# Performance work log

Measured on AMD Instinct MI355X. Metric: run time of the kernel, lower is better.

## Reference

```python
import jax, jax.numpy as jnp
import numpy as np

N = 32768      # total nodes (512 graphs x 64 padded nodes)
E = 262144     # edges (avg degree 8)
F_IN = 74      # atom feature dim
D0 = 128       # dim_embedding
D1 = 256       # hidden feats
B = 512        # batch_size (graphs)
NPG = 64       # nodes per graph
EPS = 1e-5     # BatchNorm1d eps


def setup_inputs() -> dict:
    key = jax.random.key(0)
    ks = jax.random.split(key, 8)
    def rn(k, shape, s=0.05):
        return jax.random.normal(k, shape, jnp.float32) * s
    # init_transform weight [D0, F_IN]; padding=True zeroes the last row
    W_init = rn(ks[0], (D0, F_IN)).at[-1].set(0.0)
    return {
        "node_feats": jax.random.normal(ks[1], (N, F_IN), jnp.float32),
        "W_init": W_init,
        "gcn_w1": rn(ks[2], (D0, D1)), "gcn_b1": jnp.zeros((D1,), jnp.float32),
        "res_w1": rn(ks[3], (D1, D0)), "res_b1": jnp.zeros((D1,), jnp.float32),
        "bn_g1": jnp.ones((D1,), jnp.float32), "bn_b1": jnp.zeros((D1,), jnp.float32),
        "gcn_w2": rn(ks[4], (D1, D1)), "gcn_b2": jnp.zeros((D1,), jnp.float32),
        "bn_g2": jnp.ones((D1,), jnp.float32), "bn_b2": jnp.zeros((D1,), jnp.float32),
        "edge_src": jax.random.randint(ks[5], (E,), 0, N),
        "edge_dst": jax.random.randint(ks[6], (E,), 0, N),
    }


def _agg(x, src, dst):
    # DGL GraphConv norm='both': D_out^{-1/2} gather-scatter D_in^{-1/2}, degrees clamped to >= 1
    ones = jnp.ones((src.shape[0],), x.dtype)
    deg_out = jnp.clip(jax.ops.segment_sum(ones, src, num_segments=N), 1.0)
    deg_in = jnp.clip(jax.ops.segment_sum(ones, dst, num_segments=N), 1.0)
    xs = x * jax.lax.rsqrt(deg_out)[:, None]
    agg = jax.ops.segment_sum(xs[src], dst, num_segments=N)  # [N, d]
    return agg * jax.lax.rsqrt(deg_in)[:, None]


def _bn(x, g, b):
    # BatchNorm1d training-mode: batch stats over node axis, biased var
    m = x.mean(0)
    v = x.var(0)
    return (x - m) * jax.lax.rsqrt(v + EPS) * g + b


def reference(node_feats, W_init, gcn_w1, gcn_b1, res_w1, res_b1, bn_g1, bn_b1,
              gcn_w2, gcn_b2, bn_g2, bn_b2, edge_src, edge_dst):
    h = node_feats @ W_init.T  # [N, D0]
    # layer 1: residual Linear 128->256, GCN(aggregate then weight, since in<out), GELU, BN
    res = h @ res_w1.T + res_b1
    g = jax.nn.gelu(_agg(h, edge_src, edge_dst) @ gcn_w1 + gcn_b1, approximate=False)
    h = _bn(g + res, bn_g1, bn_b1)
    # layer 2: Identity residual
    g = jax.nn.gelu(_agg(h, edge_src, edge_dst) @ gcn_w2 + gcn_b2, approximate=False)
    h = _bn(g + h, bn_g2, bn_b2)
    return h.reshape(B, NPG, D1)
```

## Files before the change

### kernel.cpp

```cpp
#include <hip/hip_runtime.h>
#include <hip/hip_bf16.h>
#include <math.h>

#define N_NODES 32768
#define E_EDGES 262144
#define F_INF   74
#define KP      96
#define D0      128
#define D1      256
#define BN_EPS  1e-5f
#define RBLK    1024

#if __has_builtin(__builtin_amdgcn_cvt_pk_f32_fp8)
#define HW_FP8 1
#else
#define HW_FP8 0
#endif

typedef float f32x4 __attribute__((ext_vector_type(4)));
typedef float f32x2 __attribute__((ext_vector_type(2)));
typedef short s16x8 __attribute__((ext_vector_type(8)));

__device__ __forceinline__ float b2f(ushort h) { return __uint_as_float(((unsigned)h) << 16); }
__device__ __forceinline__ ushort f2b(float f) {
    unsigned u = __float_as_uint(f);
    return (ushort)((u + 0x7FFFu + ((u >> 16) & 1u)) >> 16);
}
__device__ __forceinline__ unsigned char f2q(float f) {
    unsigned u = __float_as_uint(f * 7.52316384526264005e-37f);
    unsigned s = (u >> 24) & 0x80u;
    int r = (int)(((u & 0x7fffffffu) + 0x80000u) >> 20);
    r = r > 126 ? 126 : r;
    return (unsigned char)(s | (unsigned)r);
}
__device__ __forceinline__ float q2f(unsigned x) {
    unsigned fb = ((x & 0x80u) << 24) | ((x & 0x7fu) << 20);
    return __uint_as_float(fb) * 1.32922799578491587e+36f;
}
__device__ __forceinline__ void acc8(float* a, uint2 v, float c) {
#if HW_FP8
    f32x2 p;
    p = __builtin_amdgcn_cvt_pk_f32_fp8((int)v.x, false); a[0] += p[0] * c; a[1] += p[1] * c;
    p = __builtin_amdgcn_cvt_pk_f32_fp8((int)v.x, true);  a[2] += p[0] * c; a[3] += p[1] * c;
    p = __builtin_amdgcn_cvt_pk_f32_fp8((int)v.y, false); a[4] += p[0] * c; a[5] += p[1] * c;
    p = __builtin_amdgcn_cvt_pk_f32_fp8((int)v.y, true);  a[6] += p[0] * c; a[7] += p[1] * c;
#else
    unsigned d;
    d = v.x; a[0] += q2f(d & 255u) * c; a[1] += q2f((d >> 8) & 255u) * c;
             a[2] += q2f((d >> 16) & 255u) * c; a[3] += q2f(d >> 24) * c;
    d = v.y; a[4] += q2f(d & 255u) * c; a[5] += q2f((d >> 8) & 255u) * c;
             a[6] += q2f((d >> 16) & 255u) * c; a[7] += q2f(d >> 24) * c;
#endif
}
__device__ __forceinline__ float gelu_exact(float x) {
    return 0.5f * x * (1.0f + erff(x * 0.70710678118654752440f));
}


__global__ void k_front_a(const int* __restrict__ src, const int* __restrict__ dst,
                          int* __restrict__ deg,
                          const float* __restrict__ nf, const float* __restrict__ Wi,
                          const float* __restrict__ w1, const float* __restrict__ rw,
                          const float* __restrict__ w2,
                          ushort* __restrict__ nfB, ushort* __restrict__ WTB,
                          ushort* __restrict__ WB1, ushort* __restrict__ RWB,
                          ushort* __restrict__ WB2) {
    int bid = blockIdx.x;
    int tid = threadIdx.x;
    if (bid < 1024) {
        int e = bid * 256 + tid;
        atomicAdd(&deg[src[e]], 1);
        atomicAdd(&deg[N_NODES + dst[e]], 1);
        return;
    }
    int idx = (bid - 1024) * 256 + tid;
    {
        int n = idx / KP, k = idx - n * KP;
        nfB[idx] = (k < F_INF) ? f2b(nf[n * F_INF + k]) : (ushort)0;
    }
    if (idx < D0 * KP) {
        int c = idx / KP, k = idx - c * KP;
        WTB[idx] = (k < F_INF) ? f2b(Wi[c * F_INF + k]) : (ushort)0;
    }
    if (idx < D1 * D0) {
        int n = idx >> 7, k = idx & 127;
        WB1[idx] = f2b(w1[k * D1 + n]);
        RWB[idx] = f2b(rw[idx]);
    }
    if (idx < D1 * D1) {
        int n = idx >> 8, k = idx & 255;
        WB2[idx] = f2b(w2[k * D1 + n]);
    }
}

__global__ __launch_bounds__(1024) void k_scan(const int* __restrict__ deg,
                                               int* __restrict__ row_off,
                                               float* __restrict__ rsq_out,
                                               float* __restrict__ rsq_in,
                                               int* __restrict__ cursor) {
    __shared__ int part[1024];
    int t = threadIdx.x;
    int base = t * 32;
    int loc[32];
    int s = 0;
    #pragma unroll
    for (int i = 0; i < 32; i++) { loc[i] = s; s += deg[N_NODES + base + i]; }
    part[t] = s;
    #pragma unroll
    for (int i = 0; i < 32; i++) {
        int n = base + i;
        int d_o = deg[n];           if (d_o < 1) d_o = 1;
        int d_i = deg[N_NODES + n]; if (d_i < 1) d_i = 1;
        rsq_out[n] = 1.0f / sqrtf((float)d_o);
        rsq_in[n]  = 1.0f / sqrtf((float)d_i);
        cursor[n] = 0;
    }
    __syncthreads();
    for (int off = 1; off < 1024; off <<= 1) {
        int v = 0;
        if (t >= off) v = part[t - off];
        __syncthreads();
        if (t >= off) part[t] += v;
        __syncthreads();
    }
    int pre = (t == 0) ? 0 : part[t - 1];
    #pragma unroll
    for (int i = 0; i < 32; i++) row_off[base + i] = pre + loc[i];
    if (t == 1023) row_off[N_NODES] = part[1023];
}


__global__ __launch_bounds__(512) void k_front_b(
    const int* __restrict__ src, const int* __restrict__ dst,
    const int* __restrict__ row_off, const float* __restrict__ rsq_out,
    int* __restrict__ cursor, int2* __restrict__ csr,
    const ushort* __restrict__ nfB, const ushort* __restrict__ WTB,
    ushort* __restrict__ h0) {
    int bid = blockIdx.x;
    int tid = threadIdx.x;
    if (bid < 512) {
        int e = bid * 512 + tid;
        int d = dst[e];
        int s = src[e];
        int slot = atomicAdd(&cursor[d], 1);
        int pos = row_off[d] + slot;
        csr[pos] = make_int2(s, __float_as_int(rsq_out[s]));
        return;
    }
    int b2 = bid - 512;
    int w = tid >> 6, lane = tid & 63, m = lane & 15, g4 = lane >> 4;
    int col = w * 16 + m;
    int rbase = b2 * 16;
    s16x8 B[3], A[3];
    #pragma unroll
    for (int j = 0; j < 3; j++)
        B[j] = *reinterpret_cast<const s16x8*>(&WTB[(size_t)col * KP + j * 32 + g4 * 8]);
    #pragma unroll
    for (int j = 0; j < 3; j++)
        A[j] = *reinterpret_cast<const s16x8*>(&nfB[(size_t)(rbase + m) * KP + j * 32 + g4 * 8]);
    f32x4 acc = (f32x4){0.f, 0.f, 0.f, 0.f};
    #pragma unroll
    for (int j = 0; j < 3; j++)
        acc = __builtin_amdgcn_mfma_f32_16x16x32_bf16(A[j], B[j], acc, 0, 0, 0);
    #pragma unroll
    for (int r = 0; r < 4; r++)
        h0[(size_t)(rbase + g4 * 4 + r) * D0 + col] = f2b(acc[r]);
}


__global__ __launch_bounds__(512) void k_layer1f(
    const ushort* __restrict__ h0B, const float* __restrict__ rsq_in,
    const int* __restrict__ row_off, const int2* __restrict__ csr,
    const ushort* __restrict__ WB1, const ushort* __restrict__ RWB,
    const float* __restrict__ b1, const float* __restrict__ rb,
    ushort* __restrict__ t1B, unsigned char* __restrict__ t1Q,
    float* __restrict__ partials) {
    __shared__ ushort sA[32 * 128];
    int tid = threadIdx.x;
    int rbase = blockIdx.x * 32;
    {
        int nloc = tid >> 4;
        int half = (tid >> 3) & 1;
        int node = rbase + nloc;
        int f = (tid & 7) * 8;
        int beg = row_off[node], end = row_off[node + 1];
        float a0[8], a1[8];
        #pragma unroll
        for (int j = 0; j < 8; j++) { a0[j] = 0.f; a1[j] = 0.f; }
        int e = beg + half;
        for (; e + 6 < end; e += 8) {
            int2 r0 = csr[e], r1 = csr[e + 2], r2 = csr[e + 4], r3 = csr[e + 6];
            float c0 = __int_as_float(r0.y), c1 = __int_as_float(r1.y);
            float c2 = __int_as_float(r2.y), c3 = __int_as_float(r3.y);
            s16x8 v00 = *reinterpret_cast<const s16x8*>(&h0B[(size_t)r0.x * D0 + f]);
            s16x8 v01 = *reinterpret_cast<const s16x8*>(&h0B[(size_t)r0.x * D0 + f + 64]);
            s16x8 v10 = *reinterpret_cast<const s16x8*>(&h0B[(size_t)r1.x * D0 + f]);
            s16x8 v11 = *reinterpret_cast<const s16x8*>(&h0B[(size_t)r1.x * D0 + f + 64]);
            s16x8 v20 = *reinterpret_cast<const s16x8*>(&h0B[(size_t)r2.x * D0 + f]);
            s16x8 v21 = *reinterpret_cast<const s16x8*>(&h0B[(size_t)r2.x * D0 + f + 64]);
            s16x8 v30 = *reinterpret_cast<const s16x8*>(&h0B[(size_t)r3.x * D0 + f]);
            s16x8 v31 = *reinterpret_cast<const s16x8*>(&h0B[(size_t)r3.x * D0 + f + 64]);
            #pragma unroll
            for (int j = 0; j < 8; j++) {
                a0[j] += b2f((ushort)v00[j]) * c0 + b2f((ushort)v10[j]) * c1 +
                         b2f((ushort)v20[j]) * c2 + b2f((ushort)v30[j]) * c3;
                a1[j] += b2f((ushort)v01[j]) * c0 + b2f((ushort)v11[j]) * c1 +
                         b2f((ushort)v21[j]) * c2 + b2f((ushort)v31[j]) * c3;
            }
        }
        for (; e < end; e += 2) {
            int2 r = csr[e];
            float sc = __int_as_float(r.y);
            s16x8 v0 = *reinterpret_cast<const s16x8*>(&h0B[(size_t)r.x * D0 + f]);
            s16x8 v1 = *reinterpret_cast<const s16x8*>(&h0B[(size_t)r.x * D0 + f + 64]);
            #pragma unroll
            for (int j = 0; j < 8; j++) {
                a0[j] += b2f((ushort)v0[j]) * sc;
                a1[j] += b2f((ushort)v1[j]) * sc;
            }
        }
        #pragma unroll
        for (int j = 0; j < 8; j++) {
            a0[j] += __shfl_xor(a0[j], 8);
            a1[j] += __shfl_xor(a1[j], 8);
        }
        if (half == 0) {
            float si = rsq_in[node];
            s16x8 o0, o1;
            #pragma unroll
            for (int j = 0; j < 8; j++) {
                o0[j] = (short)f2b(a0[j] * si);
                o1[j] = (short)f2b(a1[j] * si);
            }
            int swz = (nloc & 15) << 4;
            int x0 = f * 2;
            *reinterpret_cast<s16x8*>(((char*)sA) + nloc * 256 + (x0 ^ swz)) = o0;
            *reinterpret_cast<s16x8*>(((char*)sA) + nloc * 256 + ((x0 + 128) ^ swz)) = o1;
        }
    }
    __syncthreads();
    int w = tid >> 6, lane = tid & 63, m = lane & 15, g4 = lane >> 4;
    int cb = w * 32;
    s16x8 BG[2][4], BR[2][4];
    #pragma unroll
    for (int nt = 0; nt < 2; nt++)
        #pragma unroll
        for (int j = 0; j < 4; j++) {
            BG[nt][j] = *reinterpret_cast<const s16x8*>(&WB1[(size_t)(cb + nt * 16 + m) * D0 + j * 32 + g4 * 8]);
            BR[nt][j] = *reinterpret_cast<const s16x8*>(&RWB[(size_t)(cb + nt * 16 + m) * D0 + j * 32 + g4 * 8]);
        }
    float bg[2], brv[2];
    #pragma unroll
    for (int nt = 0; nt < 2; nt++) {
        bg[nt]  = b1[cb + nt * 16 + m];
        brv[nt] = rb[cb + nt * 16 + m];
    }
    float ps[2] = {0.f, 0.f}, pq[2] = {0.f, 0.f};
    #pragma unroll
    for (int rt = 0; rt < 2; rt++) {
        int row = rt * 16 + m;
        s16x8 aA[4], aH[4];
        #pragma unroll
        for (int j = 0; j < 4; j++) {
            int boff = row * 256 + (((j * 4 + g4) * 16) ^ ((row & 15) << 4));
            aA[j] = *reinterpret_cast<const s16x8*>(((const char*)sA) + boff);
            aH[j] = *reinterpret_cast<const s16x8*>(&h0B[(size_t)(rbase + row) * D0 + j * 32 + g4 * 8]);
        }
        f32x4 accG[2], accR[2];
        #pragma unroll
        for (int nt = 0; nt < 2; nt++) {
            accG[nt] = (f32x4){0.f, 0.f, 0.f, 0.f};
            accR[nt] = (f32x4){0.f, 0.f, 0.f, 0.f};
        }
        #pragma unroll
        for (int j = 0; j < 4; j++)
            #pragma unroll
            for (int nt = 0; nt < 2; nt++) {
                accG[nt] = __builtin_amdgcn_mfma_f32_16x16x32_bf16(aA[j], BG[nt][j], accG[nt], 0, 0, 0);
                accR[nt] = __builtin_amdgcn_mfma_f32_16x16x32_bf16(aH[j], BR[nt][j], accR[nt], 0, 0, 0);
            }
        #pragma unroll
        for (int nt = 0; nt < 2; nt++) {
            int col = cb + nt * 16 + m;
            #pragma unroll
            for (int r = 0; r < 4; r++) {
                int orow = rbase + rt * 16 + g4 * 4 + r;
                float v = gelu_exact(accG[nt][r] + bg[nt]) + accR[nt][r] + brv[nt];
                t1B[(size_t)orow * D1 + col] = f2b(v);
                t1Q[(size_t)orow * D1 + col] = f2q(v);
                ps[nt] += v; pq[nt] += v * v;
            }
        }
    }
    #pragma unroll
    for (int nt = 0; nt < 2; nt++) {
        float s = ps[nt], q = pq[nt];
        s += __shfl_xor(s, 16); s += __shfl_xor(s, 32);
        q += __shfl_xor(q, 16); q += __shfl_xor(q, 32);
        if (g4 == 0) {
            int col = cb + nt * 16 + m;
            partials[(size_t)col * RBLK + blockIdx.x] = s;
            partials[(size_t)(256 + col) * RBLK + blockIdx.x] = q;
        }
    }
}


__global__ __launch_bounds__(1024) void k_layer2f(
    const ushort* __restrict__ t1B, const unsigned char* __restrict__ t1Q,
    const float* __restrict__ sc1, const float* __restrict__ sh1,
    const float* __restrict__ rsq_in,
    const int* __restrict__ row_off, const int2* __restrict__ csr,
    const ushort* __restrict__ WB2, const float* __restrict__ b2,
    ushort* __restrict__ t2B, float* __restrict__ partials) {
    __shared__ ushort sA[32 * 256];
    int tid = threadIdx.x;
    int rbase = blockIdx.x * 32;
    {
        int nloc = tid >> 5;
        int half = (tid >> 4) & 1;
        int node = rbase + nloc;
        int f0 = (tid & 15) * 8;
        int beg = row_off[node], end = row_off[node + 1];
        float a0[8], a1[8];
        #pragma unroll
        for (int j = 0; j < 8; j++) { a0[j] = 0.f; a1[j] = 0.f; }
        float ssum = 0.f;
        int e = beg + half;
        for (; e + 6 < end; e += 8) {
            int2 r0 = csr[e], r1 = csr[e + 2], r2 = csr[e + 4], r3 = csr[e + 6];
            float c0 = __int_as_float(r0.y), c1 = __int_as_float(r1.y);
            float c2 = __int_as_float(r2.y), c3 = __int_as_float(r3.y);
            uint2 qa0 = *reinterpret_cast<const uint2*>(&t1Q[(size_t)r0.x * D1 + f0]);
            uint2 qb0 = *reinterpret_cast<const uint2*>(&t1Q[(size_t)r0.x * D1 + f0 + 128]);
            uint2 qa1 = *reinterpret_cast<const uint2*>(&t1Q[(size_t)r1.x * D1 + f0]);
            uint2 qb1 = *reinterpret_cast<const uint2*>(&t1Q[(size_t)r1.x * D1 + f0 + 128]);
            uint2 qa2 = *reinterpret_cast<const uint2*>(&t1Q[(size_t)r2.x * D1 + f0]);
            uint2 qb2 = *reinterpret_cast<const uint2*>(&t1Q[(size_t)r2.x * D1 + f0 + 128]);
            uint2 qa3 = *reinterpret_cast<const uint2*>(&t1Q[(size_t)r3.x * D1 + f0]);
            uint2 qb3 = *reinterpret_cast<const uint2*>(&t1Q[(size_t)r3.x * D1 + f0 + 128]);
            ssum += c0 + c1 + c2 + c3;
            acc8(a0, qa0, c0); acc8(a1, qb0, c0);
            acc8(a0, qa1, c1); acc8(a1, qb1, c1);
            acc8(a0, qa2, c2); acc8(a1, qb2, c2);
            acc8(a0, qa3, c3); acc8(a1, qb3, c3);
        }
        for (; e < end; e += 2) {
            int2 r = csr[e];
            float sc = __int_as_float(r.y);
            uint2 qa = *reinterpret_cast<const uint2*>(&t1Q[(size_t)r.x * D1 + f0]);
            uint2 qb = *reinterpret_cast<const uint2*>(&t1Q[(size_t)r.x * D1 + f0 + 128]);
            ssum += sc;
            acc8(a0, qa, sc); acc8(a1, qb, sc);
        }
        #pragma unroll
        for (int j = 0; j < 8; j++) {
            a0[j] += __shfl_xor(a0[j], 16);
            a1[j] += __shfl_xor(a1[j], 16);
        }
        ssum += __shfl_xor(ssum, 16);
        if (half == 0) {
            float si = rsq_in[node];
            s16x8 o0, o1;
            #pragma unroll
            for (int j = 0; j < 8; j++) {
                o0[j] = (short)f2b((sc1[f0 + j] * a0[j] + sh1[f0 + j] * ssum) * si);
                o1[j] = (short)f2b((sc1[f0 + 128 + j] * a1[j] + sh1[f0 + 128 + j] * ssum) * si);
            }
            int swz = (nloc & 15) << 4;
            int b0 = nloc * 512 + ((f0 * 2) ^ swz);
            int b1_ = nloc * 512 + (((f0 + 128) * 2) ^ swz);
            *reinterpret_cast<s16x8*>(((char*)sA) + b0) = o0;
            *reinterpret_cast<s16x8*>(((char*)sA) + b1_) = o1;
        }
    }
    __syncthreads();
    int w = tid >> 6, lane = tid & 63, m = lane & 15, g4 = lane >> 4;
    int col = w * 16 + m;
    ushort rres[2][4];
    #pragma unroll
    for (int rt = 0; rt < 2; rt++)
        #pragma unroll
        for (int r = 0; r < 4; r++)
            rres[rt][r] = t1B[(size_t)(rbase + rt * 16 + g4 * 4 + r) * D1 + col];
    s16x8 BG[8];
    #pragma unroll
    for (int j = 0; j < 8; j++)
        BG[j] = *reinterpret_cast<const s16x8*>(&WB2[(size_t)col * D1 + j * 32 + g4 * 8]);
    float bg = b2[col], a1c = sc1[col], s1c = sh1[col];
    float ps = 0.f, pq = 0.f;
    #pragma unroll
    for (int rt = 0; rt < 2; rt++) {
        int row = rt * 16 + m;
        s16x8 aA[8];
        #pragma unroll
        for (int j = 0; j < 8; j++) {
            int boff = row * 512 + (((j * 4 + g4) * 16) ^ ((row & 15) << 4));
            aA[j] = *reinterpret_cast<const s16x8*>(((const char*)sA) + boff);
        }
        f32x4 acc = (f32x4){0.f, 0.f, 0.f, 0.f};
        #pragma unroll
        for (int j = 0; j < 8; j++)
            acc = __builtin_amdgcn_mfma_f32_16x16x32_bf16(aA[j], BG[j], acc, 0, 0, 0);
        #pragma unroll
        for (int r = 0; r < 4; r++) {
            int orow = rbase + rt * 16 + g4 * 4 + r;
            float h1v = fmaf(b2f(rres[rt][r]), a1c, s1c);
            float v = gelu_exact(acc[r] + bg) + h1v;
            t2B[(size_t)orow * D1 + col] = f2b(v);
            ps += v; pq += v * v;
        }
    }
    ps += __shfl_xor(ps, 16); ps += __shfl_xor(ps, 32);
    pq += __shfl_xor(pq, 16); pq += __shfl_xor(pq, 32);
    if (g4 == 0) {
        partials[(size_t)col * RBLK + blockIdx.x] = ps;
        partials[(size_t)(256 + col) * RBLK + blockIdx.x] = pq;
    }
}


__global__ __launch_bounds__(256) void k_reduce(
    const float* __restrict__ partials, const float* __restrict__ g,
    const float* __restrict__ b, float* __restrict__ sc, float* __restrict__ sh) {
    int c = blockIdx.x;
    int t = threadIdx.x;
    const float* ps = partials + (size_t)c * RBLK;
    const float* pq = partials + (size_t)(256 + c) * RBLK;
    float s = ps[t] + ps[t + 256] + ps[t + 512] + ps[t + 768];
    float q = pq[t] + pq[t + 256] + pq[t + 512] + pq[t + 768];
    __shared__ float Ls[256], Lq[256];
    Ls[t] = s; Lq[t] = q;
    __syncthreads();
    for (int o = 128; o > 0; o >>= 1) {
        if (t < o) { Ls[t] += Ls[t + o]; Lq[t] += Lq[t + o]; }
        __syncthreads();
    }
    if (t == 0) {
        float m = Ls[0] * (1.0f / (float)N_NODES);
        float var = Lq[0] * (1.0f / (float)N_NODES) - m * m;
        float a = g[c] / sqrtf(var + BN_EPS);
        sc[c] = a;
        sh[c] = b[c] - m * a;
    }
}


__global__ __launch_bounds__(256) void k_apply(
    const ushort* __restrict__ t2B, const float* __restrict__ sc,
    const float* __restrict__ sh, float* __restrict__ out) {
    int idx = blockIdx.x * 256 + threadIdx.x;
    size_t base = (size_t)idx * 8;
    int c = (int)(base & 255);
    s16x8 v = *reinterpret_cast<const s16x8*>(&t2B[base]);
    float4 o0, o1;
    o0.x = fmaf(b2f((ushort)v[0]), sc[c + 0], sh[c + 0]);
    o0.y = fmaf(b2f((ushort)v[1]), sc[c + 1], sh[c + 1]);
    o0.z = fmaf(b2f((ushort)v[2]), sc[c + 2], sh[c + 2]);
    o0.w = fmaf(b2f((ushort)v[3]), sc[c + 3], sh[c + 3]);
    o1.x = fmaf(b2f((ushort)v[4]), sc[c + 4], sh[c + 4]);
    o1.y = fmaf(b2f((ushort)v[5]), sc[c + 5], sh[c + 5]);
    o1.z = fmaf(b2f((ushort)v[6]), sc[c + 6], sh[c + 6]);
    o1.w = fmaf(b2f((ushort)v[7]), sc[c + 7], sh[c + 7]);
    *reinterpret_cast<float4*>(&out[base]) = o0;
    *reinterpret_cast<float4*>(&out[base + 4]) = o1;
}


static inline size_t align256(size_t x) { return (x + 255) & ~(size_t)255; }

extern "C" void kernel_launch(void* const* d_in, const int* in_sizes, int n_in,
                              void* d_out, int out_size, void* d_ws, size_t ws_size,
                              hipStream_t stream) {
    const float* node_feats = (const float*)d_in[0];
    const float* W_init     = (const float*)d_in[1];
    const float* gcn_w1     = (const float*)d_in[2];
    const float* gcn_b1     = (const float*)d_in[3];
    const float* res_w1     = (const float*)d_in[4];
    const float* res_b1     = (const float*)d_in[5];
    const float* bn_g1      = (const float*)d_in[6];
    const float* bn_b1      = (const float*)d_in[7];
    const float* gcn_w2     = (const float*)d_in[8];
    const float* gcn_b2     = (const float*)d_in[9];
    const float* bn_g2      = (const float*)d_in[10];
    const float* bn_b2      = (const float*)d_in[11];
    const int*   edge_src   = (const int*)d_in[12];
    const int*   edge_dst   = (const int*)d_in[13];
    float* out = (float*)d_out;

    char* p = (char*)d_ws;
    size_t off = 0;
    auto take = [&](size_t bytes) { void* r = p + off; off += align256(bytes); return r; };

    ushort* h0B   = (ushort*)take((size_t)N_NODES * D0 * 2);
    ushort* t1B   = (ushort*)take((size_t)N_NODES * D1 * 2);
    unsigned char* t1Q = (unsigned char*)take((size_t)N_NODES * D1);
    ushort* t2B   = (ushort*)take((size_t)N_NODES * D1 * 2);
    ushort* nfB   = (ushort*)take((size_t)N_NODES * KP * 2);
    ushort* WTB   = (ushort*)take((size_t)D0 * KP * 2);
    ushort* WB1   = (ushort*)take((size_t)D1 * D0 * 2);
    ushort* RWB   = (ushort*)take((size_t)D1 * D0 * 2);
    ushort* WB2   = (ushort*)take((size_t)D1 * D1 * 2);
    float*  part1 = (float*)take((size_t)2 * 256 * RBLK * 4);
    float*  part2 = (float*)take((size_t)2 * 256 * RBLK * 4);
    float*  sc1   = (float*)take(256 * 4);
    float*  sh1   = (float*)take(256 * 4);
    float*  sc2   = (float*)take(256 * 4);
    float*  sh2   = (float*)take(256 * 4);
    float*  rsq_out = (float*)take((size_t)N_NODES * 4);
    float*  rsq_in  = (float*)take((size_t)N_NODES * 4);
    int*    degi    = (int*)take((size_t)2 * N_NODES * 4);
    int*    cursor  = (int*)take((size_t)N_NODES * 4);
    int*    row_off = (int*)take((size_t)(N_NODES + 2) * 4);
    int2*   csr     = (int2*)take((size_t)E_EDGES * 8);

    hipMemsetAsync(degi, 0, (size_t)2 * N_NODES * 4, stream);

    k_front_a<<<1024 + (N_NODES * KP) / 256, 256, 0, stream>>>(
        edge_src, edge_dst, degi, node_feats, W_init, gcn_w1, res_w1, gcn_w2,
        nfB, WTB, WB1, RWB, WB2);

    k_scan<<<1, 1024, 0, stream>>>(degi, row_off, rsq_out, rsq_in, cursor);

    k_front_b<<<512 + N_NODES / 16, 512, 0, stream>>>(
        edge_src, edge_dst, row_off, rsq_out, cursor, csr, nfB, WTB, h0B);

    k_layer1f<<<RBLK, 512, 0, stream>>>(h0B, rsq_in, row_off, csr,
                                        WB1, RWB, gcn_b1, res_b1, t1B, t1Q, part1);
    k_reduce<<<256, 256, 0, stream>>>(part1, bn_g1, bn_b1, sc1, sh1);

    k_layer2f<<<RBLK, 1024, 0, stream>>>(t1B, t1Q, sc1, sh1, rsq_in, row_off, csr,
                                         WB2, gcn_b2, t2B, part2);
    k_reduce<<<256, 256, 0, stream>>>(part2, bn_g2, bn_b2, sc2, sh2);

    k_apply<<<(N_NODES * D1 / 8) / 256, 256, 0, stream>>>(t2B, sc2, sh2, out);
}
```

Measured before the change: 202.4 us.

## Restructure layer-2 neighbor gather to one node per half-wave with shuffled CSR

The layer-2 aggregation changes its thread mapping. Before, two 16-lane halves split a node's edges and each lane covered two 8-feature slices. Now 32 lanes each own one 8-feature slice of the full 256-wide row. Up to 32 CSR entries are loaded once per group and broadcast with shuffles, and gathers are issued in batches of 8 independent loads. This removes the cross-half shuffle reduction and the serialized CSR loads while raising memory-level parallelism. In exchange, degrees that are not a multiple of 8 cost padded dummy loads of row 0 with zero weight, and degrees above 32 fall back to a serial tail loop.

After: 198.9 us. No clear change (-1.7%).

```diff
diff --git a/kernel.cpp b/kernel.cpp
--- a/kernel.cpp
+++ b/kernel.cpp
@@ -318,61 +318,50 @@
     int rbase = blockIdx.x * 32;
     {
         int nloc = tid >> 5;
-        int half = (tid >> 4) & 1;
+        int l32 = tid & 31;
         int node = rbase + nloc;
-        int f0 = (tid & 15) * 8;
+        int f0 = l32 * 8;
         int beg = row_off[node], end = row_off[node + 1];
-        float a0[8], a1[8];
-        #pragma unroll
-        for (int j = 0; j < 8; j++) { a0[j] = 0.f; a1[j] = 0.f; }
+        int deg = end - beg;
+        int grp = (tid & 63) & 32;
+        float a[8];
+        #pragma unroll
+        for (int j = 0; j < 8; j++) a[j] = 0.f;
         float ssum = 0.f;
-        int e = beg + half;
-        for (; e + 6 < end; e += 8) {
-            int2 r0 = csr[e], r1 = csr[e + 2], r2 = csr[e + 4], r3 = csr[e + 6];
-            float c0 = __int_as_float(r0.y), c1 = __int_as_float(r1.y);
-            float c2 = __int_as_float(r2.y), c3 = __int_as_float(r3.y);
-            uint2 qa0 = *reinterpret_cast<const uint2*>(&t1Q[(size_t)r0.x * D1 + f0]);
-            uint2 qb0 = *reinterpret_cast<const uint2*>(&t1Q[(size_t)r0.x * D1 + f0 + 128]);
-            uint2 qa1 = *reinterpret_cast<const uint2*>(&t1Q[(size_t)r1.x * D1 + f0]);
-            uint2 qb1 = *reinterpret_cast<const uint2*>(&t1Q[(size_t)r1.x * D1 + f0 + 128]);
-            uint2 qa2 = *reinterpret_cast<const uint2*>(&t1Q[(size_t)r2.x * D1 + f0]);
-            uint2 qb2 = *reinterpret_cast<const uint2*>(&t1Q[(size_t)r2.x * D1 + f0 + 128]);
-            uint2 qa3 = *reinterpret_cast<const uint2*>(&t1Q[(size_t)r3.x * D1 + f0]);
-            uint2 qb3 = *reinterpret_cast<const uint2*>(&t1Q[(size_t)r3.x * D1 + f0 + 128]);
-            ssum += c0 + c1 + c2 + c3;
-            acc8(a0, qa0, c0); acc8(a1, qb0, c0);
-            acc8(a0, qa1, c1); acc8(a1, qb1, c1);
-            acc8(a0, qa2, c2); acc8(a1, qb2, c2);
-            acc8(a0, qa3, c3); acc8(a1, qb3, c3);
-        }
-        for (; e < end; e += 2) {
+        int2 my = (l32 < deg) ? csr[beg + l32] : make_int2(0, 0);
+        int nb = deg < 32 ? deg : 32;
+        for (int kb = 0; kb < nb; kb += 8) {
+            int s[8]; float c[8];
+            #pragma unroll
+            for (int k2 = 0; k2 < 8; k2++) {
+                s[k2] = __shfl(my.x, grp + kb + k2);
+                c[k2] = __int_as_float(__shfl(my.y, grp + kb + k2));
+            }
+            uint2 q[8];
+            #pragma unroll
+            for (int k2 = 0; k2 < 8; k2++)
+                q[k2] = *reinterpret_cast<const uint2*>(&t1Q[(size_t)s[k2] * D1 + f0]);
+            #pragma unroll
+            for (int k2 = 0; k2 < 8; k2++) {
+                acc8(a, q[k2], c[k2]);
+                ssum += c[k2];
+            }
+        }
+        for (int e = beg + 32; e < end; e++) {
             int2 r = csr[e];
             float sc = __int_as_float(r.y);
-            uint2 qa = *reinterpret_cast<const uint2*>(&t1Q[(size_t)r.x * D1 + f0]);
-            uint2 qb = *reinterpret_cast<const uint2*>(&t1Q[(size_t)r.x * D1 + f0 + 128]);
+            uint2 q = *reinterpret_cast<const uint2*>(&t1Q[(size_t)r.x * D1 + f0]);
             ssum += sc;
-            acc8(a0, qa, sc); acc8(a1, qb, sc);
-        }
-        #pragma unroll
-        for (int j = 0; j < 8; j++) {
-            a0[j] += __shfl_xor(a0[j], 16);
-            a1[j] += __shfl_xor(a1[j], 16);
-        }
-        ssum += __shfl_xor(ssum, 16);
-        if (half == 0) {
-            float si = rsq_in[node];
-            s16x8 o0, o1;
-            #pragma unroll
-            for (int j = 0; j < 8; j++) {
-                o0[j] = (short)f2b((sc1[f0 + j] * a0[j] + sh1[f0 + j] * ssum) * si);
-                o1[j] = (short)f2b((sc1[f0 + 128 + j] * a1[j] + sh1[f0 + 128 + j] * ssum) * si);
-            }
-            int swz = (nloc & 15) << 4;
-            int b0 = nloc * 512 + ((f0 * 2) ^ swz);
-            int b1_ = nloc * 512 + (((f0 + 128) * 2) ^ swz);
-            *reinterpret_cast<s16x8*>(((char*)sA) + b0) = o0;
-            *reinterpret_cast<s16x8*>(((char*)sA) + b1_) = o1;
-        }
+            acc8(a, q, sc);
+        }
+        float si = rsq_in[node];
+        s16x8 o;
+        #pragma unroll
+        for (int j = 0; j < 8; j++)
+            o[j] = (short)f2b((sc1[f0 + j] * a[j] + sh1[f0 + j] * ssum) * si);
+        int swz = (nloc & 15) << 4;
+        int boff = nloc * 512 + ((f0 * 2) ^ swz);
+        *reinterpret_cast<s16x8*>(((char*)sA) + boff) = o;
     }
     __syncthreads();
     int w = tid >> 6, lane = tid & 63, m = lane & 15, g4 = lane >> 4;
```
